# Performance work log

Measured on AMD Instinct MI355X. Metric: run time of the kernel, lower is better.

Reference implementation:

```python
import jax, jax.numpy as jnp
import numpy as np

D = 896      # mm_hidden_size
H = 8        # num heads
HD = D // H  # head dim = 112
M = 8        # num_memory_tokens
P = 196      # patch_size
EPS = 1e-12


def _layernorm(x, g, b):
    mu = jnp.mean(x, axis=-1, keepdims=True)
    var = jnp.mean(jnp.square(x - mu), axis=-1, keepdims=True)
    return (x - mu) * jax.lax.rsqrt(var + EPS) * g + b


def setup_inputs() -> dict:
    key = jax.random.key(0)
    ks = jax.random.split(key, 12)
    F = 32
    s = 0.02
    return {
        "image_features": jax.random.normal(ks[0], (F, P, D), jnp.float32),
        "initial_memory": jax.random.normal(ks[1], (M, P, D), jnp.float32),
        "qW": jax.random.normal(ks[2], (D, D), jnp.float32) * s,
        "qb": jnp.zeros((D,), jnp.float32),
        "kW": jax.random.normal(ks[3], (D, D), jnp.float32) * s,
        "kb": jnp.zeros((D,), jnp.float32),
        "vW": jax.random.normal(ks[4], (D, D), jnp.float32) * s,
        "vb": jnp.zeros((D,), jnp.float32),
        "oW": jax.random.normal(ks[5], (D, D), jnp.float32) * s,
        "ob": jnp.zeros((D,), jnp.float32),
        "ln1_g": jnp.ones((D,), jnp.float32),
        "ln1_b": jnp.zeros((D,), jnp.float32),
        "mW": jax.random.normal(ks[6], (D, 4 * D), jnp.float32) * s,
        "mb": jnp.zeros((4 * D,), jnp.float32),
        "pW": jax.random.normal(ks[7], (4 * D, D), jnp.float32) * s,
        "pb": jnp.zeros((D,), jnp.float32),
        "ln2_g": jnp.ones((D,), jnp.float32),
        "ln2_b": jnp.zeros((D,), jnp.float32),
    }


def reference(image_features, initial_memory, qW, qb, kW, kb, vW, vb,
              oW, ob, ln1_g, ln1_b, mW, mb, pW, pb, ln2_g, ln2_b):
    F = image_features.shape[0]
    Lq = M * P            # 1568 query tokens
    Lk = F * P            # kv tokens
    mem = initial_memory.reshape(1, Lq, D)      # [1, Lq, D]
    img = image_features.reshape(1, Lk, D)      # [1, Lk, D]

    def heads(x, L):
        return x.reshape(1, L, H, HD).transpose(0, 2, 1, 3)  # [1,H,L,hd]

    q = heads(mem @ qW + qb, Lq)
    k = heads(img @ kW + kb, Lk)
    v = heads(img @ vW + vb, Lk)

    scores = jnp.einsum('bhqd,bhkd->bhqk', q, k) / np.sqrt(HD).astype(jnp.float32)
    probs = jax.nn.softmax(scores, axis=-1)                  # [1,H,Lq,Lk]
    ctx = jnp.einsum('bhqk,bhkd->bhqd', probs, v)
    ctx = ctx.transpose(0, 2, 1, 3).reshape(1, Lq, D)

    # residual + layernorm epilogue of Attention
    attn_out = _layernorm(ctx @ oW + ob + mem, ln1_g, ln1_b)

    # MLP -> residual + layernorm
    hidden = jax.nn.relu(attn_out @ mW + mb)                 # [1, Lq, 4D]
    out = _layernorm(hidden @ pW + pb + attn_out, ln2_g, ln2_b)

    # frame attention scores: sum over heads and query tokens, avg per frame
    attn_sum = probs.sum(axis=(1, 2))[0]                     # [Lk]
    frame_scores = attn_sum.reshape(F, P).mean(axis=1)       # [F]

    final_memory = out.reshape(M, P, D)
    return final_memory, frame_scores
```

## Files before the change

### kernel.cpp

```cpp
#include <hip/hip_runtime.h>
#include <hip/hip_bf16.h>
#include <math.h>

#define TP_D   896
#define TP_H   8
#define TP_HD  112
#define TP_LQ  1568
#define TP_LK  6272
#define TP_D4  3584
#define TP_F   32
#define TP_P   196

typedef unsigned short u16;
typedef float f32x4 __attribute__((ext_vector_type(4)));
typedef __bf16 bf16x8 __attribute__((ext_vector_type(8)));

__device__ inline float bf2f(u16 u) {
    return __uint_as_float(((unsigned int)u) << 16);
}
__device__ inline u16 f2bf(float f) {
    unsigned int x = __float_as_uint(f);
    unsigned int lsb = (x >> 16) & 1u;
    x += 0x7fffu + lsb;
    return (u16)(x >> 16);
}
__device__ inline ushort4 pack4(float a, float b, float c, float d) {
    return make_ushort4(f2bf(a), f2bf(b), f2bf(c), f2bf(d));
}
__device__ inline int pidx(int row, int col) {
    return row * 128 + (col ^ ((row & 7) << 3));
}

__global__ void cast_f32_bf16(const float* __restrict__ src, u16* __restrict__ dst, int n) {
    int i = (blockIdx.x * blockDim.x + threadIdx.x) * 4;
    if (i + 3 < n) {
        float4 v = *(const float4*)(src + i);
        *(ushort4*)(dst + i) = pack4(v.x, v.y, v.z, v.w);
    } else {
        for (; i < n; ++i) dst[i] = f2bf(src[i]);
    }
}

__global__ void cast_div_bf16(const float* __restrict__ src, const float* __restrict__ l,
                              u16* __restrict__ dst) {
    int i = (blockIdx.x * 256 + threadIdx.x) * 4;
    if (i >= TP_LQ * TP_D) return;
    int q = i / TP_D;
    int col = i - q * TP_D;
    int h = col / TP_HD;
    float inv = 1.f / l[h * TP_LQ + q];
    float4 v = *(const float4*)(src + i);
    *(ushort4*)(dst + i) = pack4(v.x * inv, v.y * inv, v.z * inv, v.w * inv);
}

__global__ void transpose_cast(const float* __restrict__ src, u16* __restrict__ dst, int R, int C) {
    __shared__ float t[32][33];
    int bx = blockIdx.x * 32;
    int by = blockIdx.y * 32;
    int tx = threadIdx.x, ty = threadIdx.y;
#pragma unroll
    for (int j = 0; j < 4; ++j)
        t[ty + j * 8][tx] = src[(size_t)(by + ty + j * 8) * C + bx + tx];
    __syncthreads();
#pragma unroll
    for (int j = 0; j < 4; ++j)
        dst[(size_t)(bx + ty + j * 8) * R + by + tx] = f2bf(t[tx][ty + j * 8]);
}

struct GemmParams {
    const u16* A;  long long aZ; int lda;
    const u16* Bt; long long bZ; int ldb;
    int M, N, K;
    const float* bias;
    float* outF;
    u16* outB; long long cZ; int ldc;
    float scale;
    int hbase;
    int relu;
    int kc;
};

#define LDS_STRIDE 56

template <int MODE>
__global__ __launch_bounds__(256, 2) void gemm_bf16(GemmParams p) {
    __shared__ u16 lsA[128 * LDS_STRIDE];
    __shared__ u16 lsB[128 * LDS_STRIDE];

    const int tid = threadIdx.x;
    const int z = blockIdx.z;
    const u16* A;
    const u16* Bt;
    if (MODE == 6) {
        A  = p.A  + (size_t)z * p.kc;
        Bt = p.Bt + (size_t)z * p.kc;
    } else {
        A  = p.A  + (size_t)z * p.aZ;
        Bt = p.Bt + (size_t)z * p.bZ;
    }
    const int m0 = blockIdx.y * 128;
    const int n0 = blockIdx.x * 128;

    const int lane = tid & 63;
    const int w = tid >> 6;
    const int wm = (w >> 1) * 64, wn = (w & 1) * 64;
    const int c = lane & 15, q = lane >> 4;

    f32x4 acc[4][4];
#pragma unroll
    for (int i = 0; i < 4; ++i)
#pragma unroll
        for (int j = 0; j < 4; ++j) acc[i][j] = 0.f;

    const int r0 = tid >> 2;
    const int c8 = (tid & 3) * 8;
    int arow0 = m0 + r0;      if (arow0 >= p.M) arow0 = p.M - 1;
    int arow1 = m0 + r0 + 64; if (arow1 >= p.M) arow1 = p.M - 1;
    int brow0 = n0 + r0;      if (brow0 >= p.N) brow0 = p.N - 1;
    int brow1 = n0 + r0 + 64; if (brow1 >= p.N) brow1 = p.N - 1;
    const u16* a0 = A  + (size_t)arow0 * p.lda + c8;
    const u16* a1 = A  + (size_t)arow1 * p.lda + c8;
    const u16* b0 = Bt + (size_t)brow0 * p.ldb + c8;
    const u16* b1 = Bt + (size_t)brow1 * p.ldb + c8;

    const int KT = (p.K + 31) >> 5;
    for (int kt = 0; kt < KT; ++kt) {
        const int k0 = kt << 5;
        const bool valid = (k0 + c8 + 8) <= p.K;
        uint4 zv = make_uint4(0, 0, 0, 0);
        uint4 va0 = valid ? *(const uint4*)(a0 + k0) : zv;
        uint4 va1 = valid ? *(const uint4*)(a1 + k0) : zv;
        uint4 vb0 = valid ? *(const uint4*)(b0 + k0) : zv;
        uint4 vb1 = valid ? *(const uint4*)(b1 + k0) : zv;
        *(uint4*)(&lsA[r0 * LDS_STRIDE + c8])        = va0;
        *(uint4*)(&lsA[(r0 + 64) * LDS_STRIDE + c8]) = va1;
        *(uint4*)(&lsB[r0 * LDS_STRIDE + c8])        = vb0;
        *(uint4*)(&lsB[(r0 + 64) * LDS_STRIDE + c8]) = vb1;
        __syncthreads();

        bf16x8 af[4], bfv[4];
#pragma unroll
        for (int mi = 0; mi < 4; ++mi)
            af[mi] = *(const bf16x8*)(&lsA[(wm + mi * 16 + c) * LDS_STRIDE + q * 8]);
#pragma unroll
        for (int ni = 0; ni < 4; ++ni)
            bfv[ni] = *(const bf16x8*)(&lsB[(wn + ni * 16 + c) * LDS_STRIDE + q * 8]);
#pragma unroll
        for (int mi = 0; mi < 4; ++mi)
#pragma unroll
            for (int ni = 0; ni < 4; ++ni)
                acc[mi][ni] = __builtin_amdgcn_mfma_f32_16x16x32_bf16(af[mi], bfv[ni], acc[mi][ni], 0, 0, 0);
        __syncthreads();
    }

    if (MODE == 7) {
#pragma unroll
        for (int ni = 0; ni < 4; ++ni) {
            const int col = n0 + wn + ni * 16 + c;
            const float bv = p.bias[col];
#pragma unroll
            for (int mi = 0; mi < 4; ++mi) {
                const int mbase = m0 + wm + mi * 16 + q * 4;
                f32x4 a = acc[mi][ni];
                *(ushort4*)(p.outB + (size_t)col * p.ldc + mbase) =
                    pack4(a[0] + bv, a[1] + bv, a[2] + bv, a[3] + bv);
            }
        }
        return;
    }

#pragma unroll
    for (int mi = 0; mi < 4; ++mi) {
#pragma unroll
        for (int r = 0; r < 4; ++r) {
            const int row = m0 + wm + mi * 16 + q * 4 + r;
            if (row >= p.M) continue;
#pragma unroll
            for (int ni = 0; ni < 4; ++ni) {
                const int col = n0 + wn + ni * 16 + c;
                float v = acc[mi][ni][r];
                if (MODE == 4) {
                    v += p.bias[col];
                    if (p.relu) v = v > 0.f ? v : 0.f;
                    p.outB[(size_t)row * p.ldc + col] = f2bf(v);
                } else if (MODE == 6) {
                    atomicAdd(&p.outF[(size_t)row * p.ldc + col], v);
                }
            }
        }
    }
}

__global__ __launch_bounds__(256, 2) void attn_fused(
        const u16* __restrict__ Qf, const u16* __restrict__ Kf,
        const u16* __restrict__ Vtf, u16* __restrict__ E,
        float* __restrict__ lsum, float* __restrict__ ctxF, float scale) {
    __shared__ u16 lsQ[128 * 128];
    __shared__ u16 lsB[128 * 40];
    __shared__ u16 lsP[128 * 128];

    const int ks  = blockIdx.x;
    const int m0  = blockIdx.y * 128;
    const int h   = blockIdx.z;
    const int tid = threadIdx.x;
    const int lane = tid & 63, w = tid >> 6;
    const int wm = (w >> 1) * 64, wn = (w & 1) * 64;
    const int c = lane & 15, q = lane >> 4;

    {
        const int row = tid >> 1;
        const int half = (tid & 1) * 64;
        int qrow = m0 + row; if (qrow > TP_LQ - 1) qrow = TP_LQ - 1;
        const u16* src = Qf + (size_t)qrow * TP_D + h * TP_HD;
#pragma unroll
        for (int j = 0; j < 8; ++j) {
            int col = half + j * 8;
            uint4 v = make_uint4(0, 0, 0, 0);
            if (col + 8 <= TP_HD) v = *(const uint4*)(src + col);
            *(uint4*)(&lsQ[pidx(row, col)]) = v;
        }
    }

    const int r0 = tid >> 2;
    const int c8 = (tid & 3) * 8;
    const int keybase = ks * 896;

    f32x4 acc_pv[4][4];
#pragma unroll
    for (int i = 0; i < 4; ++i)
#pragma unroll
        for (int j = 0; j < 4; ++j) acc_pv[i][j] = 0.f;
    float rs[4] = {0.f, 0.f, 0.f, 0.f};

    for (int kb = 0; kb < 7; ++kb) {
        const int kblk = keybase + kb * 128;
        f32x4 acc_s[4][4];
#pragma unroll
        for (int i = 0; i < 4; ++i)
#pragma unroll
            for (int j = 0; j < 4; ++j) acc_s[i][j] = 0.f;

#pragma unroll
        for (int kt = 0; kt < 4; ++kt) {
            const int k0 = kt * 32;
            const bool valid = (k0 + c8 + 8) <= TP_HD;
            uint4 zv = make_uint4(0, 0, 0, 0);
            uint4 vb0 = valid ? *(const uint4*)(Kf + (size_t)(kblk + r0) * TP_D + h * TP_HD + k0 + c8) : zv;
            uint4 vb1 = valid ? *(const uint4*)(Kf + (size_t)(kblk + r0 + 64) * TP_D + h * TP_HD + k0 + c8) : zv;
            __syncthreads();
            *(uint4*)(&lsB[r0 * 40 + c8])        = vb0;
            *(uint4*)(&lsB[(r0 + 64) * 40 + c8]) = vb1;
            __syncthreads();
            bf16x8 af[4], bfv[4];
#pragma unroll
            for (int mi = 0; mi < 4; ++mi)
                af[mi] = *(const bf16x8*)(&lsQ[pidx(wm + mi * 16 + c, k0 + q * 8)]);
#pragma unroll
            for (int ni = 0; ni < 4; ++ni)
                bfv[ni] = *(const bf16x8*)(&lsB[(wn + ni * 16 + c) * 40 + q * 8]);
#pragma unroll
            for (int mi = 0; mi < 4; ++mi)
#pragma unroll
                for (int ni = 0; ni < 4; ++ni)
                    acc_s[mi][ni] = __builtin_amdgcn_mfma_f32_16x16x32_bf16(bfv[ni], af[mi], acc_s[mi][ni], 0, 0, 0);
        }

        __syncthreads();
#pragma unroll
        for (int mi = 0; mi < 4; ++mi) {
            const int prow = wm + mi * 16 + c;
            const int qr = m0 + prow;
            const bool qv = qr < TP_LQ;
            float rp = 0.f;
#pragma unroll
            for (int ni = 0; ni < 4; ++ni) {
                float e0, e1, e2, e3;
                {
                    f32x4 a = acc_s[mi][ni];
                    e0 = __expf(fminf(a[0] * scale, 30.f));
                    e1 = __expf(fminf(a[1] * scale, 30.f));
                    e2 = __expf(fminf(a[2] * scale, 30.f));
                    e3 = __expf(fminf(a[3] * scale, 30.f));
                }
                rp += (e0 + e1) + (e2 + e3);
                ushort4 pk = pack4(e0, e1, e2, e3);
                const int kcol = wn + ni * 16 + q * 4;
                if (qv)
                    *(ushort4*)(E + ((size_t)h * TP_LQ + qr) * TP_LK + kblk + kcol) = pk;
                *(ushort4*)(&lsP[pidx(prow, kcol)]) = pk;
            }
            rs[mi] += rp;
        }

#pragma unroll
        for (int kt = 0; kt < 4; ++kt) {
            const int kk = kblk + kt * 32 + c8;
            int d0 = r0;
            int d1 = r0 + 64; if (d1 > TP_HD - 1) d1 = TP_HD - 1;
            uint4 vb0 = *(const uint4*)(Vtf + ((size_t)h * TP_HD + d0) * TP_LK + kk);
            uint4 vb1 = *(const uint4*)(Vtf + ((size_t)h * TP_HD + d1) * TP_LK + kk);
            __syncthreads();
            *(uint4*)(&lsB[r0 * 40 + c8])        = vb0;
            *(uint4*)(&lsB[(r0 + 64) * 40 + c8]) = vb1;
            __syncthreads();
            bf16x8 ap[4], bv[4];
#pragma unroll
            for (int mi = 0; mi < 4; ++mi)
                ap[mi] = *(const bf16x8*)(&lsP[pidx(wm + mi * 16 + c, kt * 32 + q * 8)]);
#pragma unroll
            for (int ni = 0; ni < 4; ++ni)
                bv[ni] = *(const bf16x8*)(&lsB[(wn + ni * 16 + c) * 40 + q * 8]);
#pragma unroll
            for (int mi = 0; mi < 4; ++mi)
#pragma unroll
                for (int ni = 0; ni < 4; ++ni)
                    acc_pv[mi][ni] = __builtin_amdgcn_mfma_f32_16x16x32_bf16(ap[mi], bv[ni], acc_pv[mi][ni], 0, 0, 0);
        }
    }

#pragma unroll
    for (int mi = 0; mi < 4; ++mi) {
        float rp = rs[mi];
        rp += __shfl_xor(rp, 16, 64);
        rp += __shfl_xor(rp, 32, 64);
        const int qr = m0 + wm + mi * 16 + c;
        if (q == 0 && qr < TP_LQ) atomicAdd(&lsum[h * TP_LQ + qr], rp);
    }
#pragma unroll
    for (int mi = 0; mi < 4; ++mi) {
#pragma unroll
        for (int r = 0; r < 4; ++r) {
            const int qr = m0 + wm + mi * 16 + q * 4 + r;
            if (qr >= TP_LQ) continue;
#pragma unroll
            for (int ni = 0; ni < 4; ++ni) {
                const int d = wn + ni * 16 + c;
                if (d < TP_HD)
                    atomicAdd(&ctxF[(size_t)qr * TP_D + h * TP_HD + d], acc_pv[mi][ni][r]);
            }
        }
    }
}

__global__ void colsum_kernel(const u16* __restrict__ E, const float* __restrict__ l,
                              float* __restrict__ colsum, int nrows) {
    int c4 = blockIdx.x * 256 + threadIdx.x;
    if (c4 >= TP_LK / 4) return;
    int chunk = (nrows + gridDim.y - 1) / gridDim.y;
    int r0 = blockIdx.y * chunk;
    int r1 = r0 + chunk; if (r1 > nrows) r1 = nrows;
    float a0 = 0.f, a1 = 0.f, a2 = 0.f, a3 = 0.f;
    for (int r = r0; r < r1; ++r) {
        float inv = 1.f / l[r];
        ushort4 u = ((const ushort4*)(E + (size_t)r * TP_LK))[c4];
        a0 += bf2f(u.x) * inv; a1 += bf2f(u.y) * inv;
        a2 += bf2f(u.z) * inv; a3 += bf2f(u.w) * inv;
    }
    atomicAdd(&colsum[4 * c4 + 0], a0);
    atomicAdd(&colsum[4 * c4 + 1], a1);
    atomicAdd(&colsum[4 * c4 + 2], a2);
    atomicAdd(&colsum[4 * c4 + 3], a3);
}

__global__ __launch_bounds__(256) void layernorm_rows(const float* __restrict__ x,
        const float* __restrict__ bias, const float* __restrict__ res,
        const float* __restrict__ g, const float* __restrict__ b,
        float* __restrict__ outF, u16* __restrict__ outB) {
    const int tid = threadIdx.x;
    const float* xr = x + (size_t)blockIdx.x * TP_D;
    const float* rr = res + (size_t)blockIdx.x * TP_D;
    float v[4];
#pragma unroll
    for (int i = 0; i < 4; ++i) {
        int idx = tid + i * 256;
        v[i] = (idx < TP_D) ? (xr[idx] + bias[idx] + rr[idx]) : 0.f;
    }
    float s = v[0] + v[1] + v[2] + v[3];
    __shared__ float red[4];
#pragma unroll
    for (int o = 32; o > 0; o >>= 1) s += __shfl_xor(s, o, 64);
    if ((tid & 63) == 0) red[tid >> 6] = s;
    __syncthreads();
    const float mu = (red[0] + red[1] + red[2] + red[3]) * (1.f / TP_D);
    __syncthreads();
    float ss = 0.f;
#pragma unroll
    for (int i = 0; i < 4; ++i) {
        int idx = tid + i * 256;
        if (idx < TP_D) { float d = v[i] - mu; ss += d * d; }
    }
#pragma unroll
    for (int o = 32; o > 0; o >>= 1) ss += __shfl_xor(ss, o, 64);
    if ((tid & 63) == 0) red[tid >> 6] = ss;
    __syncthreads();
    const float var = (red[0] + red[1] + red[2] + red[3]) * (1.f / TP_D);
    const float rs = rsqrtf(var + 1e-12f);
    float* of = outF + (size_t)blockIdx.x * TP_D;
    u16* obp = outB ? outB + (size_t)blockIdx.x * TP_D : nullptr;
#pragma unroll
    for (int i = 0; i < 4; ++i) {
        int idx = tid + i * 256;
        if (idx < TP_D) {
            float y = (v[i] - mu) * rs * g[idx] + b[idx];
            of[idx] = y;
            if (obp) obp[idx] = f2bf(y);
        }
    }
}

__global__ void frame_scores_kernel(const float* __restrict__ colsum, float* __restrict__ out) {
    const int tid = threadIdx.x;
    float v = (tid < TP_P) ? colsum[blockIdx.x * TP_P + tid] : 0.f;
    __shared__ float red[4];
#pragma unroll
    for (int o = 32; o > 0; o >>= 1) v += __shfl_xor(v, o, 64);
    if ((tid & 63) == 0) red[tid >> 6] = v;
    __syncthreads();
    if (tid == 0) out[blockIdx.x] = (red[0] + red[1] + red[2] + red[3]) * (1.f / TP_P);
}

extern "C" void kernel_launch(void* const* d_in, const int* in_sizes, int n_in,
                              void* d_out, int out_size, void* d_ws, size_t ws_size,
                              hipStream_t stream) {
    const float* img  = (const float*)d_in[0];
    const float* mem  = (const float*)d_in[1];
    const float* qW   = (const float*)d_in[2];
    const float* qb   = (const float*)d_in[3];
    const float* kW   = (const float*)d_in[4];
    const float* kb   = (const float*)d_in[5];
    const float* vW   = (const float*)d_in[6];
    const float* vb   = (const float*)d_in[7];
    const float* oW   = (const float*)d_in[8];
    const float* ob   = (const float*)d_in[9];
    const float* ln1g = (const float*)d_in[10];
    const float* ln1b = (const float*)d_in[11];
    const float* mW   = (const float*)d_in[12];
    const float* mb   = (const float*)d_in[13];
    const float* pW   = (const float*)d_in[14];
    const float* pb   = (const float*)d_in[15];
    const float* ln2g = (const float*)d_in[16];
    const float* ln2b = (const float*)d_in[17];
    float* out = (float*)d_out;

    char* base = (char*)d_ws;
    size_t off = 0;
    auto take = [&](size_t nbytes) -> void* {
        void* p = base + off;
        off += (nbytes + 255) & ~(size_t)255;
        return p;
    };

    u16* imgB  = (u16*)take((size_t)TP_LK * TP_D * 2);
    u16* memB  = (u16*)take((size_t)TP_LQ * TP_D * 2);
    u16* qWt   = (u16*)take((size_t)TP_D * TP_D * 2);
    u16* kWt   = (u16*)take((size_t)TP_D * TP_D * 2);
    u16* vWt   = (u16*)take((size_t)TP_D * TP_D * 2);
    u16* oWt   = (u16*)take((size_t)TP_D * TP_D * 2);
    u16* mWt   = (u16*)take((size_t)TP_D * TP_D4 * 2);
    u16* pWt   = (u16*)take((size_t)TP_D * TP_D4 * 2);
    u16* Qf    = (u16*)take((size_t)TP_LQ * TP_D * 2);
    u16* Kf    = (u16*)take((size_t)TP_LK * TP_D * 2);
    u16* Vtf   = (u16*)take((size_t)TP_LK * TP_D * 2);
    float* ctxF  = (float*)take((size_t)TP_LQ * TP_D * 4);
    u16* ctxB  = (u16*)take((size_t)TP_LQ * TP_D * 2);
    float* pre1  = (float*)take((size_t)TP_LQ * TP_D * 4);
    float* attn  = (float*)take((size_t)TP_LQ * TP_D * 4);
    u16* attnB = (u16*)take((size_t)TP_LQ * TP_D * 2);
    u16* hidden= (u16*)take((size_t)TP_LQ * TP_D4 * 2);
    float* pre2  = (float*)take((size_t)TP_LQ * TP_D * 4);
    float* colsum= (float*)take((size_t)TP_LK * 4);
    float* lsum  = (float*)take((size_t)TP_H * TP_LQ * 4);
    u16* E     = (u16*)take((size_t)TP_H * TP_LQ * TP_LK * 2);

    cast_f32_bf16<<<(TP_LK * TP_D / 4 + 255) / 256, 256, 0, stream>>>(img, imgB, TP_LK * TP_D);
    cast_f32_bf16<<<(TP_LQ * TP_D / 4 + 255) / 256, 256, 0, stream>>>(mem, memB, TP_LQ * TP_D);
    transpose_cast<<<dim3(28, 28), dim3(32, 8), 0, stream>>>(qW, qWt, TP_D, TP_D);
    transpose_cast<<<dim3(28, 28), dim3(32, 8), 0, stream>>>(kW, kWt, TP_D, TP_D);
    transpose_cast<<<dim3(28, 28), dim3(32, 8), 0, stream>>>(vW, vWt, TP_D, TP_D);
    transpose_cast<<<dim3(28, 28), dim3(32, 8), 0, stream>>>(oW, oWt, TP_D, TP_D);
    transpose_cast<<<dim3(TP_D4 / 32, TP_D / 32), dim3(32, 8), 0, stream>>>(mW, mWt, TP_D, TP_D4);
    transpose_cast<<<dim3(TP_D / 32, TP_D4 / 32), dim3(32, 8), 0, stream>>>(pW, pWt, TP_D4, TP_D);
    hipMemsetAsync(colsum, 0, (size_t)TP_LK * 4, stream);
    hipMemsetAsync(lsum, 0, (size_t)TP_H * TP_LQ * 4, stream);
    hipMemsetAsync(ctxF, 0, (size_t)TP_LQ * TP_D * 4, stream);
    hipMemsetAsync(pre1, 0, (size_t)TP_LQ * TP_D * 4, stream);
    hipMemsetAsync(pre2, 0, (size_t)TP_LQ * TP_D * 4, stream);

    {
        GemmParams p{};
        p.A = memB; p.aZ = 0; p.lda = TP_D;
        p.Bt = qWt; p.bZ = 0; p.ldb = TP_D;
        p.M = TP_LQ; p.N = TP_D; p.K = TP_D;
        p.bias = qb; p.outB = Qf; p.ldc = TP_D; p.relu = 0;
        gemm_bf16<4><<<dim3(7, 13, 1), 256, 0, stream>>>(p);
    }
    {
        GemmParams p{};
        p.A = imgB; p.aZ = 0; p.lda = TP_D;
        p.Bt = kWt; p.bZ = 0; p.ldb = TP_D;
        p.M = TP_LK; p.N = TP_D; p.K = TP_D;
        p.bias = kb; p.outB = Kf; p.ldc = TP_D; p.relu = 0;
        gemm_bf16<4><<<dim3(7, 49, 1), 256, 0, stream>>>(p);
    }
    {
        GemmParams p{};
        p.A = imgB; p.aZ = 0; p.lda = TP_D;
        p.Bt = vWt; p.bZ = 0; p.ldb = TP_D;
        p.M = TP_LK; p.N = TP_D; p.K = TP_D;
        p.bias = vb; p.outB = Vtf; p.ldc = TP_LK;
        gemm_bf16<7><<<dim3(7, 49, 1), 256, 0, stream>>>(p);
    }

    const float scale = 0.09449111825230679f;
    attn_fused<<<dim3(7, 13, TP_H), 256, 0, stream>>>(Qf, Kf, Vtf, E, lsum, ctxF, scale);
    colsum_kernel<<<dim3(7, 224), 256, 0, stream>>>(E, lsum, colsum, TP_H * TP_LQ);
    cast_div_bf16<<<(TP_LQ * TP_D / 4 + 255) / 256, 256, 0, stream>>>(ctxF, lsum, ctxB);

    {
        GemmParams p{};
        p.A = ctxB; p.lda = TP_D;
        p.Bt = oWt; p.ldb = TP_D;
        p.M = TP_LQ; p.N = TP_D; p.K = 448; p.kc = 448;
        p.outF = pre1; p.ldc = TP_D;
        gemm_bf16<6><<<dim3(7, 13, 2), 256, 0, stream>>>(p);
    }
    layernorm_rows<<<TP_LQ, 256, 0, stream>>>(pre1, ob, mem, ln1g, ln1b, attn, attnB);

    {
        GemmParams p{};
        p.A = attnB; p.aZ = 0; p.lda = TP_D;
        p.Bt = mWt; p.bZ = 0; p.ldb = TP_D;
        p.M = TP_LQ; p.N = TP_D4; p.K = TP_D;
        p.bias = mb; p.outB = hidden; p.ldc = TP_D4; p.relu = 1;
        gemm_bf16<4><<<dim3(28, 13, 1), 256, 0, stream>>>(p);
    }
    {
        GemmParams p{};
        p.A = hidden; p.lda = TP_D4;
        p.Bt = pWt; p.ldb = TP_D4;
        p.M = TP_LQ; p.N = TP_D; p.K = 896; p.kc = 896;
        p.outF = pre2; p.ldc = TP_D;
        gemm_bf16<6><<<dim3(7, 13, 4), 256, 0, stream>>>(p);
    }
    layernorm_rows<<<TP_LQ, 256, 0, stream>>>(pre2, pb, attn, ln2g, ln2b, out, nullptr);

    frame_scores_kernel<<<TP_F, 256, 0, stream>>>(colsum, out + (size_t)TP_LQ * TP_D);
}
```

Before: 557.9 us.

## Store attention probs as fp8, keep Q in registers, shrink GEMM N-tile

The attention kernel now writes the exponentiated scores for the column-sum pass as 8-bit floats instead of bf16, halving the largest intermediate buffer's traffic. Q fragments are held in registers instead of LDS, the K/V staging buffer is double-buffered so one barrier per step is removed, and the GEMMs use a narrower 64-column N tile with higher occupancy bounds and twice the grid. The five memsets are merged into one by reordering the buffers contiguously. The fp8 encoding loses precision in the frame scores, and the narrower tiles lower data reuse per block.

```diff
diff --git a/kernel.cpp b/kernel.cpp
--- a/kernel.cpp
+++ b/kernel.cpp
@@ -26,6 +26,25 @@
 }
 __device__ inline ushort4 pack4(float a, float b, float c, float d) {
     return make_ushort4(f2bf(a), f2bf(b), f2bf(c), f2bf(d));
+}
+__device__ inline unsigned char f2fp8(float f) {
+    if (f >= 448.f) return 0x7E;
+    if (f < 0.015625f) {
+        int m = (int)(f * 512.f + 0.5f);
+        if (m >= 8) return 0x08;
+        return (unsigned char)m;
+    }
+    unsigned u = __float_as_uint(f) + 0x00080000u;
+    int e = (int)((u >> 23) & 0xFF) - 127;
+    int m = (u >> 20) & 7;
+    int E = e + 7;
+    if (E > 15) return 0x7E;
+    return (unsigned char)((E << 3) | m);
+}
+__device__ inline float fp82f(unsigned b) {
+    int E = (b >> 3) & 0xF, M = b & 7;
+    if (E == 0) return (float)M * (1.f / 512.f);
+    return __uint_as_float((unsigned)((E + 120) << 23) | ((unsigned)M << 20));
 }
 __device__ inline int pidx(int row, int col) {
     return row * 128 + (col ^ ((row & 7) << 3));
@@ -68,49 +87,44 @@
 }
 
 struct GemmParams {
-    const u16* A;  long long aZ; int lda;
-    const u16* Bt; long long bZ; int ldb;
+    const u16* A;  int lda;
+    const u16* Bt; int ldb;
     int M, N, K;
     const float* bias;
     float* outF;
-    u16* outB; long long cZ; int ldc;
-    float scale;
-    int hbase;
+    u16* outB; int ldc;
     int relu;
     int kc;
 };
 
 #define LDS_STRIDE 56
 
-template <int MODE>
-__global__ __launch_bounds__(256, 2) void gemm_bf16(GemmParams p) {
+template <int MODE, int NT>
+__global__ __launch_bounds__(256, 4) void gemm_bf16(GemmParams p) {
     __shared__ u16 lsA[128 * LDS_STRIDE];
-    __shared__ u16 lsB[128 * LDS_STRIDE];
+    __shared__ u16 lsB[NT * 32 * LDS_STRIDE];
 
     const int tid = threadIdx.x;
     const int z = blockIdx.z;
-    const u16* A;
-    const u16* Bt;
+    const u16* A  = p.A;
+    const u16* Bt = p.Bt;
     if (MODE == 6) {
-        A  = p.A  + (size_t)z * p.kc;
-        Bt = p.Bt + (size_t)z * p.kc;
-    } else {
-        A  = p.A  + (size_t)z * p.aZ;
-        Bt = p.Bt + (size_t)z * p.bZ;
+        A  += (size_t)z * p.kc;
+        Bt += (size_t)z * p.kc;
     }
     const int m0 = blockIdx.y * 128;
-    const int n0 = blockIdx.x * 128;
+    const int n0 = blockIdx.x * (NT * 32);
 
     const int lane = tid & 63;
     const int w = tid >> 6;
-    const int wm = (w >> 1) * 64, wn = (w & 1) * 64;
+    const int wm = (w >> 1) * 64, wn = (w & 1) * (16 * NT);
     const int c = lane & 15, q = lane >> 4;
 
-    f32x4 acc[4][4];
+    f32x4 acc[4][NT];
 #pragma unroll
     for (int i = 0; i < 4; ++i)
 #pragma unroll
-        for (int j = 0; j < 4; ++j) acc[i][j] = 0.f;
+        for (int j = 0; j < NT; ++j) acc[i][j] = 0.f;
 
     const int r0 = tid >> 2;
     const int c8 = (tid & 3) * 8;
@@ -131,31 +145,32 @@
         uint4 va0 = valid ? *(const uint4*)(a0 + k0) : zv;
         uint4 va1 = valid ? *(const uint4*)(a1 + k0) : zv;
         uint4 vb0 = valid ? *(const uint4*)(b0 + k0) : zv;
-        uint4 vb1 = valid ? *(const uint4*)(b1 + k0) : zv;
+        uint4 vb1 = (NT == 4 && valid) ? *(const uint4*)(b1 + k0) : zv;
         *(uint4*)(&lsA[r0 * LDS_STRIDE + c8])        = va0;
         *(uint4*)(&lsA[(r0 + 64) * LDS_STRIDE + c8]) = va1;
         *(uint4*)(&lsB[r0 * LDS_STRIDE + c8])        = vb0;
-        *(uint4*)(&lsB[(r0 + 64) * LDS_STRIDE + c8]) = vb1;
+        if (NT == 4)
+            *(uint4*)(&lsB[(r0 + 64) * LDS_STRIDE + c8]) = vb1;
         __syncthreads();
 
-        bf16x8 af[4], bfv[4];
+        bf16x8 af[4], bfv[NT];
 #pragma unroll
         for (int mi = 0; mi < 4; ++mi)
             af[mi] = *(const bf16x8*)(&lsA[(wm + mi * 16 + c) * LDS_STRIDE + q * 8]);
 #pragma unroll
-        for (int ni = 0; ni < 4; ++ni)
+        for (int ni = 0; ni < NT; ++ni)
             bfv[ni] = *(const bf16x8*)(&lsB[(wn + ni * 16 + c) * LDS_STRIDE + q * 8]);
 #pragma unroll
         for (int mi = 0; mi < 4; ++mi)
 #pragma unroll
-            for (int ni = 0; ni < 4; ++ni)
+            for (int ni = 0; ni < NT; ++ni)
                 acc[mi][ni] = __builtin_amdgcn_mfma_f32_16x16x32_bf16(af[mi], bfv[ni], acc[mi][ni], 0, 0, 0);
         __syncthreads();
     }
 
     if (MODE == 7) {
 #pragma unroll
-        for (int ni = 0; ni < 4; ++ni) {
+        for (int ni = 0; ni < NT; ++ni) {
             const int col = n0 + wn + ni * 16 + c;
             const float bv = p.bias[col];
 #pragma unroll
@@ -176,7 +191,7 @@
             const int row = m0 + wm + mi * 16 + q * 4 + r;
             if (row >= p.M) continue;
 #pragma unroll
-            for (int ni = 0; ni < 4; ++ni) {
+            for (int ni = 0; ni < NT; ++ni) {
                 const int col = n0 + wn + ni * 16 + c;
                 float v = acc[mi][ni][r];
                 if (MODE == 4) {
@@ -193,43 +208,40 @@
 
 __global__ __launch_bounds__(256, 2) void attn_fused(
         const u16* __restrict__ Qf, const u16* __restrict__ Kf,
-        const u16* __restrict__ Vtf, u16* __restrict__ E,
+        const u16* __restrict__ Vtf, unsigned char* __restrict__ E8,
         float* __restrict__ lsum, float* __restrict__ ctxF, float scale) {
-    __shared__ u16 lsQ[128 * 128];
-    __shared__ u16 lsB[128 * 40];
     __shared__ u16 lsP[128 * 128];
-
-    const int ks  = blockIdx.x;
-    const int m0  = blockIdx.y * 128;
-    const int h   = blockIdx.z;
+    __shared__ u16 lsB[2][128 * 40];
+
+    const int ks = blockIdx.x;
+    const int m0 = blockIdx.y * 128;
+    const int h  = blockIdx.z;
     const int tid = threadIdx.x;
     const int lane = tid & 63, w = tid >> 6;
     const int wm = (w >> 1) * 64, wn = (w & 1) * 64;
     const int c = lane & 15, q = lane >> 4;
 
-    {
-        const int row = tid >> 1;
-        const int half = (tid & 1) * 64;
-        int qrow = m0 + row; if (qrow > TP_LQ - 1) qrow = TP_LQ - 1;
-        const u16* src = Qf + (size_t)qrow * TP_D + h * TP_HD;
-#pragma unroll
-        for (int j = 0; j < 8; ++j) {
-            int col = half + j * 8;
-            uint4 v = make_uint4(0, 0, 0, 0);
-            if (col + 8 <= TP_HD) v = *(const uint4*)(src + col);
-            *(uint4*)(&lsQ[pidx(row, col)]) = v;
-        }
-    }
-
-    const int r0 = tid >> 2;
-    const int c8 = (tid & 3) * 8;
+    bf16x8 qf[4][4];
+#pragma unroll
+    for (int mi = 0; mi < 4; ++mi) {
+        int qr = m0 + wm + mi * 16 + c; if (qr > TP_LQ - 1) qr = TP_LQ - 1;
+        const u16* src = Qf + (size_t)qr * TP_D + h * TP_HD;
+#pragma unroll
+        for (int kt = 0; kt < 4; ++kt) {
+            int d0 = kt * 32 + q * 8;
+            if (d0 + 8 <= TP_HD) qf[mi][kt] = *(const bf16x8*)(src + d0);
+            else { union { int4 i; bf16x8 v; } u; u.i = make_int4(0, 0, 0, 0); qf[mi][kt] = u.v; }
+        }
+    }
+
+    const int r0 = tid >> 2, c8 = (tid & 3) * 8;
     const int keybase = ks * 896;
 
-    f32x4 acc_pv[4][4];
+    f32x4 apv[4][4];
 #pragma unroll
     for (int i = 0; i < 4; ++i)
 #pragma unroll
-        for (int j = 0; j < 4; ++j) acc_pv[i][j] = 0.f;
+        for (int j = 0; j < 4; ++j) apv[i][j] = 0.f;
     float rs[4] = {0.f, 0.f, 0.f, 0.f};
 
     for (int kb = 0; kb < 7; ++kb) {
@@ -247,25 +259,21 @@
             uint4 zv = make_uint4(0, 0, 0, 0);
             uint4 vb0 = valid ? *(const uint4*)(Kf + (size_t)(kblk + r0) * TP_D + h * TP_HD + k0 + c8) : zv;
             uint4 vb1 = valid ? *(const uint4*)(Kf + (size_t)(kblk + r0 + 64) * TP_D + h * TP_HD + k0 + c8) : zv;
+            u16* Bb = lsB[kt & 1];
+            *(uint4*)(&Bb[r0 * 40 + c8])        = vb0;
+            *(uint4*)(&Bb[(r0 + 64) * 40 + c8]) = vb1;
             __syncthreads();
-            *(uint4*)(&lsB[r0 * 40 + c8])        = vb0;
-            *(uint4*)(&lsB[(r0 + 64) * 40 + c8]) = vb1;
-            __syncthreads();
-            bf16x8 af[4], bfv[4];
+            bf16x8 kf[4];
+#pragma unroll
+            for (int ni = 0; ni < 4; ++ni)
+                kf[ni] = *(const bf16x8*)(&Bb[(wn + ni * 16 + c) * 40 + q * 8]);
 #pragma unroll
             for (int mi = 0; mi < 4; ++mi)
-                af[mi] = *(const bf16x8*)(&lsQ[pidx(wm + mi * 16 + c, k0 + q * 8)]);
-#pragma unroll
-            for (int ni = 0; ni < 4; ++ni)
-                bfv[ni] = *(const bf16x8*)(&lsB[(wn + ni * 16 + c) * 40 + q * 8]);
-#pragma unroll
-            for (int mi = 0; mi < 4; ++mi)
 #pragma unroll
                 for (int ni = 0; ni < 4; ++ni)
-                    acc_s[mi][ni] = __builtin_amdgcn_mfma_f32_16x16x32_bf16(bfv[ni], af[mi], acc_s[mi][ni], 0, 0, 0);
-        }
-
-        __syncthreads();
+                    acc_s[mi][ni] = __builtin_amdgcn_mfma_f32_16x16x32_bf16(kf[ni], qf[mi][kt], acc_s[mi][ni], 0, 0, 0);
+        }
+
 #pragma unroll
         for (int mi = 0; mi < 4; ++mi) {
             const int prow = wm + mi * 16 + c;
@@ -274,34 +282,34 @@
             float rp = 0.f;
 #pragma unroll
             for (int ni = 0; ni < 4; ++ni) {
-                float e0, e1, e2, e3;
-                {
-                    f32x4 a = acc_s[mi][ni];
-                    e0 = __expf(fminf(a[0] * scale, 30.f));
-                    e1 = __expf(fminf(a[1] * scale, 30.f));
-                    e2 = __expf(fminf(a[2] * scale, 30.f));
-                    e3 = __expf(fminf(a[3] * scale, 30.f));
+                f32x4 a = acc_s[mi][ni];
+                float e0 = __expf(fminf(a[0] * scale, 30.f));
+                float e1 = __expf(fminf(a[1] * scale, 30.f));
+                float e2 = __expf(fminf(a[2] * scale, 30.f));
+                float e3 = __expf(fminf(a[3] * scale, 30.f));
+                rp += (e0 + e1) + (e2 + e3);
+                const int kcol = wn + ni * 16 + q * 4;
+                *(ushort4*)(&lsP[pidx(prow, kcol)]) = pack4(e0, e1, e2, e3);
+                if (qv) {
+                    uchar4 v8;
+                    v8.x = f2fp8(e0); v8.y = f2fp8(e1);
+                    v8.z = f2fp8(e2); v8.w = f2fp8(e3);
+                    *(uchar4*)(E8 + ((size_t)h * TP_LQ + qr) * TP_LK + kblk + kcol) = v8;
                 }
-                rp += (e0 + e1) + (e2 + e3);
-                ushort4 pk = pack4(e0, e1, e2, e3);
-                const int kcol = wn + ni * 16 + q * 4;
-                if (qv)
-                    *(ushort4*)(E + ((size_t)h * TP_LQ + qr) * TP_LK + kblk + kcol) = pk;
-                *(ushort4*)(&lsP[pidx(prow, kcol)]) = pk;
             }
             rs[mi] += rp;
         }
+        __syncthreads();
 
 #pragma unroll
         for (int kt = 0; kt < 4; ++kt) {
             const int kk = kblk + kt * 32 + c8;
-            int d0 = r0;
             int d1 = r0 + 64; if (d1 > TP_HD - 1) d1 = TP_HD - 1;
-            uint4 vb0 = *(const uint4*)(Vtf + ((size_t)h * TP_HD + d0) * TP_LK + kk);
-            uint4 vb1 = *(const uint4*)(Vtf + ((size_t)h * TP_HD + d1) * TP_LK + kk);
-            __syncthreads();
-            *(uint4*)(&lsB[r0 * 40 + c8])        = vb0;
-            *(uint4*)(&lsB[(r0 + 64) * 40 + c8]) = vb1;
+            uint4 wv0 = *(const uint4*)(Vtf + ((size_t)(h * TP_HD + r0)) * TP_LK + kk);
+            uint4 wv1 = *(const uint4*)(Vtf + ((size_t)(h * TP_HD + d1)) * TP_LK + kk);
+            u16* Bb = lsB[kt & 1];
+            *(uint4*)(&Bb[r0 * 40 + c8])        = wv0;
+            *(uint4*)(&Bb[(r0 + 64) * 40 + c8]) = wv1;
             __syncthreads();
             bf16x8 ap[4], bv[4];
 #pragma unroll
@@ -309,12 +317,12 @@
                 ap[mi] = *(const bf16x8*)(&lsP[pidx(wm + mi * 16 + c, kt * 32 + q * 8)]);
 #pragma unroll
             for (int ni = 0; ni < 4; ++ni)
-                bv[ni] = *(const bf16x8*)(&lsB[(wn + ni * 16 + c) * 40 + q * 8]);
+                bv[ni] = *(const bf16x8*)(&Bb[(wn + ni * 16 + c) * 40 + q * 8]);
 #pragma unroll
             for (int mi = 0; mi < 4; ++mi)
 #pragma unroll
                 for (int ni = 0; ni < 4; ++ni)
-                    acc_pv[mi][ni] = __builtin_amdgcn_mfma_f32_16x16x32_bf16(ap[mi], bv[ni], acc_pv[mi][ni], 0, 0, 0);
+                    apv[mi][ni] = __builtin_amdgcn_mfma_f32_16x16x32_bf16(ap[mi], bv[ni], apv[mi][ni], 0, 0, 0);
         }
     }
 
@@ -336,13 +344,13 @@
             for (int ni = 0; ni < 4; ++ni) {
                 const int d = wn + ni * 16 + c;
                 if (d < TP_HD)
-                    atomicAdd(&ctxF[(size_t)qr * TP_D + h * TP_HD + d], acc_pv[mi][ni][r]);
+                    atomicAdd(&ctxF[(size_t)qr * TP_D + h * TP_HD + d], apv[mi][ni][r]);
             }
         }
     }
 }
 
-__global__ void colsum_kernel(const u16* __restrict__ E, const float* __restrict__ l,
+__global__ void colsum_kernel(const unsigned char* __restrict__ E8, const float* __restrict__ l,
                               float* __restrict__ colsum, int nrows) {
     int c4 = blockIdx.x * 256 + threadIdx.x;
     if (c4 >= TP_LK / 4) return;
@@ -351,10 +359,12 @@
     int r1 = r0 + chunk; if (r1 > nrows) r1 = nrows;
     float a0 = 0.f, a1 = 0.f, a2 = 0.f, a3 = 0.f;
     for (int r = r0; r < r1; ++r) {
+        unsigned u = ((const unsigned*)(E8 + (size_t)r * TP_LK))[c4];
         float inv = 1.f / l[r];
-        ushort4 u = ((const ushort4*)(E + (size_t)r * TP_LK))[c4];
-        a0 += bf2f(u.x) * inv; a1 += bf2f(u.y) * inv;
-        a2 += bf2f(u.z) * inv; a3 += bf2f(u.w) * inv;
+        a0 += fp82f(u & 255u) * inv;
+        a1 += fp82f((u >> 8) & 255u) * inv;
+        a2 += fp82f((u >> 16) & 255u) * inv;
+        a3 += fp82f((u >> 24) & 255u) * inv;
     }
     atomicAdd(&colsum[4 * c4 + 0], a0);
     atomicAdd(&colsum[4 * c4 + 1], a1);
@@ -394,14 +404,14 @@
     if ((tid & 63) == 0) red[tid >> 6] = ss;
     __syncthreads();
     const float var = (red[0] + red[1] + red[2] + red[3]) * (1.f / TP_D);
-    const float rs = rsqrtf(var + 1e-12f);
+    const float rsq = rsqrtf(var + 1e-12f);
     float* of = outF + (size_t)blockIdx.x * TP_D;
     u16* obp = outB ? outB + (size_t)blockIdx.x * TP_D : nullptr;
 #pragma unroll
     for (int i = 0; i < 4; ++i) {
         int idx = tid + i * 256;
         if (idx < TP_D) {
-            float y = (v[i] - mu) * rs * g[idx] + b[idx];
+            float y = (v[i] - mu) * rsq * g[idx] + b[idx];
             of[idx] = y;
             if (obp) obp[idx] = f2bf(y);
         }
@@ -461,16 +471,17 @@
     u16* Qf    = (u16*)take((size_t)TP_LQ * TP_D * 2);
     u16* Kf    = (u16*)take((size_t)TP_LK * TP_D * 2);
     u16* Vtf   = (u16*)take((size_t)TP_LK * TP_D * 2);
-    float* ctxF  = (float*)take((size_t)TP_LQ * TP_D * 4);
     u16* ctxB  = (u16*)take((size_t)TP_LQ * TP_D * 2);
-    float* pre1  = (float*)take((size_t)TP_LQ * TP_D * 4);
     float* attn  = (float*)take((size_t)TP_LQ * TP_D * 4);
     u16* attnB = (u16*)take((size_t)TP_LQ * TP_D * 2);
     u16* hidden= (u16*)take((size_t)TP_LQ * TP_D4 * 2);
+    unsigned char* E8 = (unsigned char*)take((size_t)TP_H * TP_LQ * TP_LK);
+    float* ctxF  = (float*)take((size_t)TP_LQ * TP_D * 4);
+    float* pre1  = (float*)take((size_t)TP_LQ * TP_D * 4);
     float* pre2  = (float*)take((size_t)TP_LQ * TP_D * 4);
     float* colsum= (float*)take((size_t)TP_LK * 4);
     float* lsum  = (float*)take((size_t)TP_H * TP_LQ * 4);
-    u16* E     = (u16*)take((size_t)TP_H * TP_LQ * TP_LK * 2);
+    size_t zlen = (char*)(lsum + TP_H * TP_LQ) - (char*)ctxF;
 
     cast_f32_bf16<<<(TP_LK * TP_D / 4 + 255) / 256, 256, 0, stream>>>(img, imgB, TP_LK * TP_D);
     cast_f32_bf16<<<(TP_LQ * TP_D / 4 + 255) / 256, 256, 0, stream>>>(mem, memB, TP_LQ * TP_D);
@@ -480,40 +491,36 @@
     transpose_cast<<<dim3(28, 28), dim3(32, 8), 0, stream>>>(oW, oWt, TP_D, TP_D);
     transpose_cast<<<dim3(TP_D4 / 32, TP_D / 32), dim3(32, 8), 0, stream>>>(mW, mWt, TP_D, TP_D4);
     transpose_cast<<<dim3(TP_D / 32, TP_D4 / 32), dim3(32, 8), 0, stream>>>(pW, pWt, TP_D4, TP_D);
-    hipMemsetAsync(colsum, 0, (size_t)TP_LK * 4, stream);
-    hipMemsetAsync(lsum, 0, (size_t)TP_H * TP_LQ * 4, stream);
-    hipMemsetAsync(ctxF, 0, (size_t)TP_LQ * TP_D * 4, stream);
-    hipMemsetAsync(pre1, 0, (size_t)TP_LQ * TP_D * 4, stream);
-    hipMemsetAsync(pre2, 0, (size_t)TP_LQ * TP_D * 4, stream);
+    hipMemsetAsync(ctxF, 0, zlen, stream);
 
     {
         GemmParams p{};
-        p.A = memB; p.aZ = 0; p.lda = TP_D;
-        p.Bt = qWt; p.bZ = 0; p.ldb = TP_D;
+        p.A = memB; p.lda = TP_D;
+        p.Bt = qWt; p.ldb = TP_D;
         p.M = TP_LQ; p.N = TP_D; p.K = TP_D;
         p.bias = qb; p.outB = Qf; p.ldc = TP_D; p.relu = 0;
-        gemm_bf16<4><<<dim3(7, 13, 1), 256, 0, stream>>>(p);
+        gemm_bf16<4, 2><<<dim3(14, 13, 1), 256, 0, stream>>>(p);
     }
     {
         GemmParams p{};
-        p.A = imgB; p.aZ = 0; p.lda = TP_D;
-        p.Bt = kWt; p.bZ = 0; p.ldb = TP_D;
+        p.A = imgB; p.lda = TP_D;
+        p.Bt = kWt; p.ldb = TP_D;
         p.M = TP_LK; p.N = TP_D; p.K = TP_D;
         p.bias = kb; p.outB = Kf; p.ldc = TP_D; p.relu = 0;
-        gemm_bf16<4><<<dim3(7, 49, 1), 256, 0, stream>>>(p);
+        gemm_bf16<4, 2><<<dim3(14, 49, 1), 256, 0, stream>>>(p);
     }
     {
         GemmParams p{};
-        p.A = imgB; p.aZ = 0; p.lda = TP_D;
-        p.Bt = vWt; p.bZ = 0; p.ldb = TP_D;
+        p.A = imgB; p.lda = TP_D;
+        p.Bt = vWt; p.ldb = TP_D;
         p.M = TP_LK; p.N = TP_D; p.K = TP_D;
         p.bias = vb; p.outB = Vtf; p.ldc = TP_LK;
-        gemm_bf16<7><<<dim3(7, 49, 1), 256, 0, stream>>>(p);
+        gemm_bf16<7, 2><<<dim3(14, 49, 1), 256, 0, stream>>>(p);
     }
 
     const float scale = 0.09449111825230679f;
-    attn_fused<<<dim3(7, 13, TP_H), 256, 0, stream>>>(Qf, Kf, Vtf, E, lsum, ctxF, scale);
-    colsum_kernel<<<dim3(7, 224), 256, 0, stream>>>(E, lsum, colsum, TP_H * TP_LQ);
+    attn_fused<<<dim3(7, 13, TP_H), 256, 0, stream>>>(Qf, Kf, Vtf, E8, lsum, ctxF, scale);
+    colsum_kernel<<<dim3(7, 224), 256, 0, stream>>>(E8, lsum, colsum, TP_H * TP_LQ);
     cast_div_bf16<<<(TP_LQ * TP_D / 4 + 255) / 256, 256, 0, stream>>>(ctxF, lsum, ctxB);
 
     {
@@ -522,17 +529,17 @@
         p.Bt = oWt; p.ldb = TP_D;
         p.M = TP_LQ; p.N = TP_D; p.K = 448; p.kc = 448;
         p.outF = pre1; p.ldc = TP_D;
-        gemm_bf16<6><<<dim3(7, 13, 2), 256, 0, stream>>>(p);
+        gemm_bf16<6, 2><<<dim3(14, 13, 2), 256, 0, stream>>>(p);
     }
     layernorm_rows<<<TP_LQ, 256, 0, stream>>>(pre1, ob, mem, ln1g, ln1b, attn, attnB);
 
     {
         GemmParams p{};
-        p.A = attnB; p.aZ = 0; p.lda = TP_D;
-        p.Bt = mWt; p.bZ = 0; p.ldb = TP_D;
+        p.A = attnB; p.lda = TP_D;
+        p.Bt = mWt; p.ldb = TP_D;
         p.M = TP_LQ; p.N = TP_D4; p.K = TP_D;
         p.bias = mb; p.outB = hidden; p.ldc = TP_D4; p.relu = 1;
-        gemm_bf16<4><<<dim3(28, 13, 1), 256, 0, stream>>>(p);
+        gemm_bf16<4, 2><<<dim3(56, 13, 1), 256, 0, stream>>>(p);
     }
     {
         GemmParams p{};
@@ -540,7 +547,7 @@
         p.Bt = pWt; p.ldb = TP_D4;
         p.M = TP_LQ; p.N = TP_D; p.K = 896; p.kc = 896;
         p.outF = pre2; p.ldc = TP_D;
-        gemm_bf16<6><<<dim3(7, 13, 4), 256, 0, stream>>>(p);
+        gemm_bf16<6, 2><<<dim3(14, 13, 4), 256, 0, stream>>>(p);
     }
     layernorm_rows<<<TP_LQ, 256, 0, stream>>>(pre2, pb, attn, ln2g, ln2b, out, nullptr);
 
```

Result: slower. 660.1 us (+18.3%).
